# Kernel optimization log

Hardware: AMD Instinct MI355X
Metric: run time of the kernel (lower is better)

## Reference

```python
import jax, jax.numpy as jnp
import numpy as np

E, H = 512, 256  # embed_dim, hidden_dim
B, SQ, SK = 2, 512, 512


def _linear_params(k, fin, fout):
    lim = 1.0 / np.sqrt(fin)
    kw, kb = jax.random.split(k)
    W = jax.random.uniform(kw, (fin, fout), minval=-lim, maxval=lim, dtype=jnp.float32)
    b = jax.random.uniform(kb, (fout,), minval=-lim, maxval=lim, dtype=jnp.float32)
    return W, b


def setup_inputs() -> dict:
    rng = jax.random.key(0)
    ks = jax.random.split(rng, 12)
    query = jax.random.normal(ks[0], (B, SQ, E), dtype=jnp.float32)
    key = jax.random.normal(ks[1], (B, SK, E), dtype=jnp.float32)
    Wqe, bqe = _linear_params(ks[2], E, H)
    Wke, bke = _linear_params(ks[3], E, H)
    W1, b1 = _linear_params(ks[4], 2 * H, H)  # importance_predictor layer 0
    W2, b2 = _linear_params(ks[5], H, H)      # layer 1
    W3, b3 = _linear_params(ks[6], H, H)      # layer 2
    Wf, bf = _linear_params(ks[7], H, 1)      # final importance logit
    Wv1, bv1 = _linear_params(ks[8], 2 * H, H)  # variance_estimator layer 0
    Wv2, bv2 = _linear_params(ks[9], H, 1)      # variance_estimator final
    return {"query": query, "key": key,
            "Wqe": Wqe, "bqe": bqe, "Wke": Wke, "bke": bke,
            "W1": W1, "b1": b1, "W2": W2, "b2": b2, "W3": W3, "b3": b3,
            "Wf": Wf, "bf": bf, "Wv1": Wv1, "bv1": bv1, "Wv2": Wv2, "bv2": bv2}


def reference(query, key, Wqe, bqe, Wke, bke, W1, b1, W2, b2, W3, b3, Wf, bf, Wv1, bv1, Wv2, bv2):
    # Encoders (dropout is identity at eval)
    qf = jax.nn.relu(jnp.einsum('bqe,eh->bqh', query, Wqe) + bqe)  # [B,Sq,H]
    kf = jax.nn.relu(jnp.einsum('bke,eh->bkh', key, Wke) + bke)    # [B,Sk,H]

    # First Linear(2H,H) on cat([q,k]) == q@W1[:H] + k@W1[H:]; broadcast over pairs
    qp = jnp.einsum('bqh,hd->bqd', qf, W1[:H])
    kp = jnp.einsum('bkh,hd->bkd', kf, W1[H:])
    h = jax.nn.relu(qp[:, :, None, :] + kp[:, None, :, :] + b1)  # [B,Sq,Sk,H]
    h = jax.nn.relu(jnp.einsum('bqkh,hd->bqkd', h, W2) + b2)
    h = jax.nn.relu(jnp.einsum('bqkh,hd->bqkd', h, W3) + b3)
    importance_logits = (jnp.einsum('bqkh,ho->bqko', h, Wf) + bf)[..., 0]  # [B,Sq,Sk]

    # Variance head: Linear(2H,H) split the same way, ReLU, Linear, Softplus
    vq = jnp.einsum('bqh,hd->bqd', qf, Wv1[:H])
    vk = jnp.einsum('bkh,hd->bkd', kf, Wv1[H:])
    v = jax.nn.relu(vq[:, :, None, :] + vk[:, None, :, :] + bv1)  # [B,Sq,Sk,H]
    estimated_variance = jax.nn.softplus((jnp.einsum('bqkh,ho->bqko', v, Wv2) + bv2)[..., 0])
    return importance_logits, estimated_variance
```

## Files before the change

kernel.cpp:

```cpp
#include <hip/hip_runtime.h>
#include <hip/hip_bf16.h>
#include <cstdint>
#include <cstddef>
#include <cstring>

#define HDIM 256
#define EDIM 512
#define NB   2
#define NSQ  512
#define NSK  512

typedef _Float16 f16x8 __attribute__((ext_vector_type(8)));
typedef _Float16 h2    __attribute__((ext_vector_type(2)));
typedef __fp16   fp16v2 __attribute__((ext_vector_type(2)));
typedef float    f32x4  __attribute__((ext_vector_type(4)));

#define OFF_W2F  0u
#define OFF_W3F  65536u
#define OFF_WQEF 131072u
#define OFF_WKEF 262144u
#define OFF_WCQ  393216u
#define OFF_WCK  524288u
#define OFF_WV2H 655360u
#define F16_WS_END_BYTES 1312768u

union U8 { f16x8 v; h2 h[4]; };

__device__ __forceinline__ ushort2 f2h2(float x, float y) {
  fp16v2 r = __builtin_amdgcn_cvt_pkrtz(x, y);
  ushort2 u;
  __builtin_memcpy(&u, &r, 4);
  return u;
}
__device__ __forceinline__ float relu_(float x) { return x > 0.f ? x : 0.f; }
__device__ __forceinline__ float softplus_(float x) {
  return fmaxf(x, 0.f) + log1pf(expf(-fabsf(x)));
}

__global__ __launch_bounds__(256) void shuffle_weights(
    const float* __restrict__ Wqe, const float* __restrict__ Wke,
    const float* __restrict__ W1,  const float* __restrict__ Wv1,
    const float* __restrict__ W2,  const float* __restrict__ W3,
    const float* __restrict__ Wv2,
    unsigned short* __restrict__ wsb)
{
  __shared__ float sW[32 * 257];
  const int bx = blockIdx.x;
  const int t = threadIdx.x;
  if (bx == 80) {
    if (t < 64) {
      float a = Wv2[t * 4 + 0], b = Wv2[t * 4 + 1];
      float c = Wv2[t * 4 + 2], d = Wv2[t * 4 + 3];
      ushort2 lo = f2h2(a, b), hi = f2h2(c, d);
      ushort4 o; o.x = lo.x; o.y = lo.y; o.z = hi.x; o.w = hi.y;
      *(ushort4*)&wsb[OFF_WV2H + t * 4] = o;
    }
    return;
  }
  const float* src; unsigned short* dst; int s; int S;
  if      (bx <  8) { src = W2;          dst = wsb + OFF_W2F;           s = bx;      S = 8;  }
  else if (bx < 16) { src = W3;          dst = wsb + OFF_W3F;           s = bx - 8;  S = 8;  }
  else if (bx < 32) { src = Wqe;         dst = wsb + OFF_WQEF;          s = bx - 16; S = 16; }
  else if (bx < 48) { src = Wke;         dst = wsb + OFF_WKEF;          s = bx - 32; S = 16; }
  else if (bx < 56) { src = W1;          dst = wsb + OFF_WCQ;           s = bx - 48; S = 8;  }
  else if (bx < 64) { src = Wv1;         dst = wsb + OFF_WCQ + 65536u;  s = bx - 56; S = 8;  }
  else if (bx < 72) { src = W1 + 65536;  dst = wsb + OFF_WCK;           s = bx - 64; S = 8;  }
  else              { src = Wv1 + 65536; dst = wsb + OFF_WCK + 65536u;  s = bx - 72; S = 8;  }

  const int kbase = s * 32;
  #pragma unroll
  for (int it = 0; it < 8; ++it) {
    const int f4 = it * 256 + t;
    const int row = f4 >> 6, c4 = (f4 & 63) * 4;
    float4 v = *(const float4*)(src + (size_t)(kbase + row) * 256 + c4);
    sW[row * 257 + c4 + 0] = v.x; sW[row * 257 + c4 + 1] = v.y;
    sW[row * 257 + c4 + 2] = v.z; sW[row * 257 + c4 + 3] = v.w;
  }
  __syncthreads();

  const int wave = t >> 6, lane = t & 63;
  const int n_in = lane & 15, k0 = (lane >> 4) * 8;
  for (int tt = wave * 4; tt < wave * 4 + 4; ++tt) {
    const int n = tt * 16 + n_in;
    float x[8];
    #pragma unroll
    for (int j = 0; j < 8; ++j) x[j] = sW[(k0 + j) * 257 + n];
    ushort2 p0 = f2h2(x[0], x[1]), p1 = f2h2(x[2], x[3]);
    ushort2 p2 = f2h2(x[4], x[5]), p3 = f2h2(x[6], x[7]);
    ushort4 lo; lo.x = p0.x; lo.y = p0.y; lo.z = p1.x; lo.w = p1.y;
    ushort4 hi; hi.x = p2.x; hi.y = p2.y; hi.z = p3.x; hi.w = p3.y;
    unsigned short* o = dst + ((size_t)(tt * S + s) * 64 + lane) * 8;
    *(ushort4*)&o[0] = lo; *(ushort4*)&o[4] = hi;
  }
}

__global__ __launch_bounds__(512) void encoder_kernel(
    const float* __restrict__ query, const float* __restrict__ key,
    const float* __restrict__ bqe,   const float* __restrict__ bke,
    const float* __restrict__ b1,    const float* __restrict__ bv1,
    const unsigned short* __restrict__ WqeF, const unsigned short* __restrict__ WkeF,
    const unsigned short* __restrict__ WcqF, const unsigned short* __restrict__ WckF,
    _Float16* __restrict__ Pq, _Float16* __restrict__ Pk)
{
  __shared__ unsigned short sX[16 * 520];
  __shared__ unsigned short sF[16 * 264];
  __shared__ float sBe[256];
  __shared__ float sBc[512];

  const int bx   = blockIdx.x;
  const int side = bx >> 8;
  const int idx  = bx & 255;
  const int rt   = idx >> 2;
  const int nh   = idx & 3;
  const int t    = threadIdx.x;

  const float* Xsrc = side ? key : query;
  const unsigned short* WeF = side ? WkeF : WqeF;
  const unsigned short* WcF = side ? WckF : WcqF;
  _Float16* P = side ? Pk : Pq;

  const int wave = t >> 6, lane = t & 63;
  const int l15 = lane & 15, q4 = lane >> 4;

  const unsigned short* aeb = WeF + ((size_t)(wave * 2) * 16 * 64 + lane) * 8;
  f16x8 afe[2][2];
  #pragma unroll
  for (int ft = 0; ft < 2; ++ft)
    afe[0][ft] = *(const f16x8*)(aeb + ft * 8192);

  {
    const int m = t >> 5, ch = t & 31;
    const float* xr = Xsrc + (size_t)(rt * 16 + m) * EDIM;
    #pragma unroll
    for (int j = 0; j < 4; ++j) {
      const int c = j * 128 + ch * 4;
      float4 v = *(const float4*)(xr + c);
      ushort2 lo = f2h2(v.x, v.y), hi = f2h2(v.z, v.w);
      ushort4 xb; xb.x = lo.x; xb.y = lo.y; xb.z = hi.x; xb.w = hi.y;
      *(ushort4*)&sX[m * 520 + c] = xb;
    }
    if (t < 256) {
      sBe[t]       = side ? bke[t] : bqe[t];
      sBc[t]       = side ? 0.f : b1[t];
      sBc[256 + t] = side ? 0.f : bv1[t];
    }
  }
  __syncthreads();

  f32x4 acc1[2];
  #pragma unroll
  for (int ft = 0; ft < 2; ++ft) acc1[ft] = (f32x4){0.f, 0.f, 0.f, 0.f};

  #pragma unroll
  for (int s = 0; s < 16; ++s) {
    if (s < 15) {
      #pragma unroll
      for (int ft = 0; ft < 2; ++ft)
        afe[(s + 1) & 1][ft] = *(const f16x8*)(aeb + ft * 8192 + (size_t)(s + 1) * 512);
    }
    f16x8 bfr = *(const f16x8*)&sX[l15 * 520 + s * 32 + q4 * 8];
    #pragma unroll
    for (int ft = 0; ft < 2; ++ft)
      acc1[ft] = __builtin_amdgcn_mfma_f32_16x16x32_f16(afe[s & 1][ft], bfr, acc1[ft], 0, 0, 0);
  }

  #pragma unroll
  for (int ft = 0; ft < 2; ++ft) {
    const int tg = wave * 2 + ft;
    const int n0 = tg * 16 + q4 * 4;
    float4 b4 = *(const float4*)&sBe[n0];
    f32x4 a = acc1[ft];
    ushort2 lo = f2h2(relu_(a[0] + b4.x), relu_(a[1] + b4.y));
    ushort2 hi = f2h2(relu_(a[2] + b4.z), relu_(a[3] + b4.w));
    ushort4 h; h.x = lo.x; h.y = lo.y; h.z = hi.x; h.w = hi.y;
    *(ushort4*)&sF[l15 * 264 + n0] = h;
  }
  __syncthreads();

  const int tg2 = nh * 8 + wave;
  const unsigned short* acb = WcF + ((size_t)tg2 * 8 * 64 + lane) * 8;
  f16x8 afc[2];
  afc[0] = *(const f16x8*)(acb);

  f32x4 acc2 = (f32x4){0.f, 0.f, 0.f, 0.f};

  #pragma unroll
  for (int s = 0; s < 8; ++s) {
    if (s < 7)
      afc[(s + 1) & 1] = *(const f16x8*)(acb + (size_t)(s + 1) * 512);
    f16x8 bfr = *(const f16x8*)&sF[l15 * 264 + s * 32 + q4 * 8];
    acc2 = __builtin_amdgcn_mfma_f32_16x16x32_f16(afc[s & 1], bfr, acc2, 0, 0, 0);
  }

  {
    const int n0 = tg2 * 16 + q4 * 4;
    float4 bc = *(const float4*)&sBc[n0];
    const int row = rt * 16 + l15;
    ushort2 lo = f2h2(acc2[0] + bc.x, acc2[1] + bc.y);
    ushort2 hi = f2h2(acc2[2] + bc.z, acc2[3] + bc.w);
    ushort4 o; o.x = lo.x; o.y = lo.y; o.z = hi.x; o.w = hi.y;
    *(ushort4*)((unsigned short*)P + (size_t)row * 512 + n0) = o;
  }
}

__global__ __launch_bounds__(512, 4) void pair_kernel(
    const _Float16* __restrict__ Pq, const _Float16* __restrict__ Pk,
    const unsigned short* __restrict__ W2F, const unsigned short* __restrict__ W3F,
    const float* __restrict__ b2, const float* __restrict__ b3,
    const float* __restrict__ Wf, const float* __restrict__ bfp,
    const unsigned short* __restrict__ Wv2H, const float* __restrict__ bv2p,
    float* __restrict__ out)
{
  __shared__ __align__(16) unsigned char smem[68608];
  unsigned short* sXH = (unsigned short*)smem;
  unsigned short* sH  = (unsigned short*)(smem + 33792);
  float* sRed = (float*)(smem + 67584);

  const int kt = blockIdx.x, qy = blockIdx.y, bz = blockIdx.z;
  const int t = threadIdx.x;
  const _Float16* qpRow = Pq + (size_t)(bz * NSQ + qy) * 512;

  const int wave = t >> 6, lane = t & 63;
  const int l15 = lane & 15, q4 = lane >> 4;
  const int mi = wave >> 2;
  const int ni = wave & 3;

  const unsigned short* a2base = W2F + ((size_t)(ni * 4) * 8 * 64 + lane) * 8;
  const unsigned short* a3base = W3F + ((size_t)(ni * 4) * 8 * 64 + lane) * 8;

  float vp0 = 0.f, vp1 = 0.f;
  {
    const int m   = t >> 3;
    const int sub = t & 7;
    const _Float16* kpRow = Pk + (size_t)(bz * NSK + kt * 64 + m) * 512;
    const f16x8 z8 = {0, 0, 0, 0, 0, 0, 0, 0};
    #pragma unroll
    for (int it = 0; it < 4; ++it) {
      const int c = it * 64 + sub * 8;
      f16x8 q8 = *(const f16x8*)(qpRow + c);
      f16x8 k8 = *(const f16x8*)(kpRow + c);
      f16x8 r  = __builtin_elementwise_max(q8 + k8, z8);
      *(f16x8*)&sXH[m * 264 + c] = r;
      f16x8 a8 = *(const f16x8*)(qpRow + 256 + c);
      f16x8 v8 = *(const f16x8*)(kpRow + 256 + c);
      U8 ar; ar.v = __builtin_elementwise_max(a8 + v8, z8);
      U8 w8; w8.v = *(const f16x8*)((const _Float16*)Wv2H + c);
      vp0 = __builtin_amdgcn_fdot2(ar.h[0], w8.h[0], vp0, false);
      vp1 = __builtin_amdgcn_fdot2(ar.h[1], w8.h[1], vp1, false);
      vp0 = __builtin_amdgcn_fdot2(ar.h[2], w8.h[2], vp0, false);
      vp1 = __builtin_amdgcn_fdot2(ar.h[3], w8.h[3], vp1, false);
    }
  }
  __syncthreads();

  f32x4 acc[4][2];
  #pragma unroll
  for (int ft = 0; ft < 4; ++ft)
    #pragma unroll
    for (int pt = 0; pt < 2; ++pt)
      acc[ft][pt] = (f32x4){0.f, 0.f, 0.f, 0.f};

  #pragma unroll
  for (int s = 0; s < 8; ++s) {
    f16x8 afd[4], bf[2];
    #pragma unroll
    for (int ft = 0; ft < 4; ++ft)
      afd[ft] = *(const f16x8*)(a2base + ft * 4096 + (size_t)s * 512);
    #pragma unroll
    for (int pt = 0; pt < 2; ++pt)
      bf[pt] = *(const f16x8*)&sXH[(mi * 32 + pt * 16 + l15) * 264 + s * 32 + q4 * 8];
    __builtin_amdgcn_s_setprio(1);
    #pragma unroll
    for (int ft = 0; ft < 4; ++ft)
      #pragma unroll
      for (int pt = 0; pt < 2; ++pt)
        acc[ft][pt] = __builtin_amdgcn_mfma_f32_16x16x32_f16(afd[ft], bf[pt], acc[ft][pt], 0, 0, 0);
    __builtin_amdgcn_s_setprio(0);
  }

  #pragma unroll
  for (int ft = 0; ft < 4; ++ft) {
    const int tg = ni * 4 + ft;
    const int n0 = tg * 16 + q4 * 4;
    float4 b4 = *(const float4*)&b2[n0];
    #pragma unroll
    for (int pt = 0; pt < 2; ++pt) {
      const int mr = mi * 32 + pt * 16 + l15;
      f32x4 a = acc[ft][pt];
      ushort2 lo = f2h2(relu_(a[0] + b4.x), relu_(a[1] + b4.y));
      ushort2 hi = f2h2(relu_(a[2] + b4.z), relu_(a[3] + b4.w));
      ushort4 h; h.x = lo.x; h.y = lo.y; h.z = hi.x; h.w = hi.y;
      *(ushort4*)&sH[mr * 264 + n0] = h;
    }
  }
  __syncthreads();

  #pragma unroll
  for (int ft = 0; ft < 4; ++ft)
    #pragma unroll
    for (int pt = 0; pt < 2; ++pt)
      acc[ft][pt] = (f32x4){0.f, 0.f, 0.f, 0.f};

  #pragma unroll
  for (int s = 0; s < 8; ++s) {
    f16x8 afd[4], bf[2];
    #pragma unroll
    for (int ft = 0; ft < 4; ++ft)
      afd[ft] = *(const f16x8*)(a3base + ft * 4096 + (size_t)s * 512);
    #pragma unroll
    for (int pt = 0; pt < 2; ++pt)
      bf[pt] = *(const f16x8*)&sH[(mi * 32 + pt * 16 + l15) * 264 + s * 32 + q4 * 8];
    __builtin_amdgcn_s_setprio(1);
    #pragma unroll
    for (int ft = 0; ft < 4; ++ft)
      #pragma unroll
      for (int pt = 0; pt < 2; ++pt)
        acc[ft][pt] = __builtin_amdgcn_mfma_f32_16x16x32_f16(afd[ft], bf[pt], acc[ft][pt], 0, 0, 0);
    __builtin_amdgcn_s_setprio(0);
  }

  {
    float v = vp0 + vp1;
    v += __shfl_xor(v, 1, 64);
    v += __shfl_xor(v, 2, 64);
    v += __shfl_xor(v, 4, 64);
    if ((t & 7) == 0) {
      const int m = t >> 3;
      const size_t o = (size_t)(bz * NSQ + qy) * NSK + kt * 64 + m;
      out[(size_t)NB * NSQ * NSK + o] = softplus_(v + bv2p[0]);
    }
  }

  {
    float p[2] = {0.f, 0.f};
    #pragma unroll
    for (int ft = 0; ft < 4; ++ft) {
      const int tg = ni * 4 + ft;
      const int n0 = tg * 16 + q4 * 4;
      float4 b4 = *(const float4*)&b3[n0];
      float4 w4 = *(const float4*)&Wf[n0];
      #pragma unroll
      for (int pt = 0; pt < 2; ++pt) {
        f32x4 a = acc[ft][pt];
        p[pt] += relu_(a[0] + b4.x) * w4.x + relu_(a[1] + b4.y) * w4.y
               + relu_(a[2] + b4.z) * w4.z + relu_(a[3] + b4.w) * w4.w;
      }
    }
    #pragma unroll
    for (int pt = 0; pt < 2; ++pt) {
      float v = p[pt];
      v += __shfl_xor(v, 16, 64);
      v += __shfl_xor(v, 32, 64);
      if (lane < 16) sRed[ni * 64 + mi * 32 + pt * 16 + lane] = v;
    }
  }
  __syncthreads();

  if (t < 64) {
    const size_t o = (size_t)(bz * NSQ + qy) * NSK + kt * 64 + t;
    float lg = bfp[0];
    #pragma unroll
    for (int w = 0; w < 4; ++w) lg += sRed[w * 64 + t];
    out[o] = lg;
  }
}

extern "C" void kernel_launch(void* const* d_in, const int* in_sizes, int n_in,
                              void* d_out, int out_size, void* d_ws, size_t ws_size,
                              hipStream_t stream)
{
  (void)in_sizes; (void)n_in; (void)out_size; (void)ws_size;
  const float* query = (const float*)d_in[0];
  const float* key   = (const float*)d_in[1];
  const float* Wqe   = (const float*)d_in[2];
  const float* bqe   = (const float*)d_in[3];
  const float* Wke   = (const float*)d_in[4];
  const float* bke   = (const float*)d_in[5];
  const float* W1    = (const float*)d_in[6];
  const float* b1    = (const float*)d_in[7];
  const float* W2    = (const float*)d_in[8];
  const float* b2    = (const float*)d_in[9];
  const float* W3    = (const float*)d_in[10];
  const float* b3    = (const float*)d_in[11];
  const float* Wf    = (const float*)d_in[12];
  const float* bf    = (const float*)d_in[13];
  const float* Wv1   = (const float*)d_in[14];
  const float* bv1   = (const float*)d_in[15];
  const float* Wv2   = (const float*)d_in[16];
  const float* bv2   = (const float*)d_in[17];

  unsigned short* wsb = (unsigned short*)d_ws;
  _Float16* Pq = (_Float16*)((char*)d_ws + F16_WS_END_BYTES);
  _Float16* Pk = Pq + (size_t)1024 * 512;
  float* out = (float*)d_out;

  shuffle_weights<<<81, 256, 0, stream>>>(Wqe, Wke, W1, Wv1, W2, W3, Wv2, wsb);
  encoder_kernel<<<512, 512, 0, stream>>>(query, key, bqe, bke, b1, bv1,
      wsb + OFF_WQEF, wsb + OFF_WKEF, wsb + OFF_WCQ, wsb + OFF_WCK, Pq, Pk);
  pair_kernel<<<dim3(NSK / 64, NSQ, NB), 512, 0, stream>>>(Pq, Pk,
      wsb + OFF_W2F, wsb + OFF_W3F, b2, b3, Wf, bf, wsb + OFF_WV2H, bv2, out);
}
```

Before: 290.2 us.

## Switch pair-kernel GEMMs to 32x32x16 MFMA with software-pipelined operand loads

The pair kernel's two 256x256 GEMM stages now use 32x32x16 f16 MFMA tiles, two per wave, instead of eight 16x16x32 tiles. The weight-repacking kernel gets a matching 32-wide fragment layout for W2/W3. Weight and LDS operand fragments are prefetched one or two k-steps ahead in a register double-buffer so loads overlap the MFMAs. Larger MFMA tiles reduce instruction count and fragment traffic per FLOP, at the cost of a different accumulator layout in the epilogue and more live registers.

```diff
diff --git a/kernel.cpp b/kernel.cpp
--- a/kernel.cpp
+++ b/kernel.cpp
@@ -14,6 +14,7 @@
 typedef _Float16 h2    __attribute__((ext_vector_type(2)));
 typedef __fp16   fp16v2 __attribute__((ext_vector_type(2)));
 typedef float    f32x4  __attribute__((ext_vector_type(4)));
+typedef float    f32x16 __attribute__((ext_vector_type(16)));
 
 #define OFF_W2F  0u
 #define OFF_W3F  65536u
@@ -79,6 +80,27 @@
   __syncthreads();
 
   const int wave = t >> 6, lane = t & 63;
+
+  if (bx < 16) {
+    const int n_in = lane & 31, kh = (lane >> 5) * 8;
+    #pragma unroll
+    for (int it = 0; it < 4; ++it) {
+      const int tt  = wave * 2 + (it >> 1);
+      const int scl = it & 1;
+      const int k0 = scl * 16 + kh;
+      float x[8];
+      #pragma unroll
+      for (int j = 0; j < 8; ++j) x[j] = sW[(k0 + j) * 257 + tt * 32 + n_in];
+      ushort2 p0 = f2h2(x[0], x[1]), p1 = f2h2(x[2], x[3]);
+      ushort2 p2 = f2h2(x[4], x[5]), p3 = f2h2(x[6], x[7]);
+      ushort4 lo; lo.x = p0.x; lo.y = p0.y; lo.z = p1.x; lo.w = p1.y;
+      ushort4 hi; hi.x = p2.x; hi.y = p2.y; hi.z = p3.x; hi.w = p3.y;
+      unsigned short* o = dst + ((size_t)(tt * 16 + (s * 2 + scl)) * 64 + lane) * 8;
+      *(ushort4*)&o[0] = lo; *(ushort4*)&o[4] = hi;
+    }
+    return;
+  }
+
   const int n_in = lane & 15, k0 = (lane >> 4) * 8;
   for (int tt = wave * 4; tt < wave * 4 + 4; ++tt) {
     const int n = tt * 16 + n_in;
@@ -221,12 +243,15 @@
   const _Float16* qpRow = Pq + (size_t)(bz * NSQ + qy) * 512;
 
   const int wave = t >> 6, lane = t & 63;
-  const int l15 = lane & 15, q4 = lane >> 4;
+  const int l31 = lane & 31, kh = lane >> 5;
   const int mi = wave >> 2;
-  const int ni = wave & 3;
-
-  const unsigned short* a2base = W2F + ((size_t)(ni * 4) * 8 * 64 + lane) * 8;
-  const unsigned short* a3base = W3F + ((size_t)(ni * 4) * 8 * 64 + lane) * 8;
+  const int nj = wave & 3;
+
+  const unsigned short* a2b = W2F + (size_t)(nj * 2) * 8192 + lane * 8;
+  const unsigned short* a3b = W3F + (size_t)(nj * 2) * 8192 + lane * 8;
+
+  f16x8 a0c = *(const f16x8*)(a2b);
+  f16x8 a1c = *(const f16x8*)(a2b + 8192);
 
   float vp0 = 0.f, vp1 = 0.f;
   {
@@ -253,70 +278,71 @@
   }
   __syncthreads();
 
-  f32x4 acc[4][2];
-  #pragma unroll
-  for (int ft = 0; ft < 4; ++ft)
-    #pragma unroll
-    for (int pt = 0; pt < 2; ++pt)
-      acc[ft][pt] = (f32x4){0.f, 0.f, 0.f, 0.f};
-
-  #pragma unroll
-  for (int s = 0; s < 8; ++s) {
-    f16x8 afd[4], bf[2];
-    #pragma unroll
-    for (int ft = 0; ft < 4; ++ft)
-      afd[ft] = *(const f16x8*)(a2base + ft * 4096 + (size_t)s * 512);
-    #pragma unroll
-    for (int pt = 0; pt < 2; ++pt)
-      bf[pt] = *(const f16x8*)&sXH[(mi * 32 + pt * 16 + l15) * 264 + s * 32 + q4 * 8];
+  const int m = mi * 32 + l31;
+  const int brow = m * 264 + kh * 8;
+
+  f32x16 acc0, acc1;
+  #pragma unroll
+  for (int i = 0; i < 16; ++i) { acc0[i] = 0.f; acc1[i] = 0.f; }
+
+  f16x8 bc = *(const f16x8*)&sXH[brow];
+  f16x8 b1f = *(const f16x8*)&sXH[brow + 16];
+
+  #pragma unroll
+  for (int sc = 0; sc < 16; ++sc) {
+    f16x8 a0n, a1n, b2n;
+    if (sc < 15) {
+      a0n = *(const f16x8*)(a2b + (size_t)(sc + 1) * 512);
+      a1n = *(const f16x8*)(a2b + 8192 + (size_t)(sc + 1) * 512);
+    }
+    if (sc < 14)
+      b2n = *(const f16x8*)&sXH[brow + (sc + 2) * 16];
     __builtin_amdgcn_s_setprio(1);
-    #pragma unroll
-    for (int ft = 0; ft < 4; ++ft)
-      #pragma unroll
-      for (int pt = 0; pt < 2; ++pt)
-        acc[ft][pt] = __builtin_amdgcn_mfma_f32_16x16x32_f16(afd[ft], bf[pt], acc[ft][pt], 0, 0, 0);
+    acc0 = __builtin_amdgcn_mfma_f32_32x32x16_f16(a0c, bc, acc0, 0, 0, 0);
+    acc1 = __builtin_amdgcn_mfma_f32_32x32x16_f16(a1c, bc, acc1, 0, 0, 0);
     __builtin_amdgcn_s_setprio(0);
-  }
-
-  #pragma unroll
-  for (int ft = 0; ft < 4; ++ft) {
-    const int tg = ni * 4 + ft;
-    const int n0 = tg * 16 + q4 * 4;
-    float4 b4 = *(const float4*)&b2[n0];
-    #pragma unroll
-    for (int pt = 0; pt < 2; ++pt) {
-      const int mr = mi * 32 + pt * 16 + l15;
-      f32x4 a = acc[ft][pt];
-      ushort2 lo = f2h2(relu_(a[0] + b4.x), relu_(a[1] + b4.y));
-      ushort2 hi = f2h2(relu_(a[2] + b4.z), relu_(a[3] + b4.w));
+    a0c = a0n; a1c = a1n; bc = b1f; b1f = b2n;
+  }
+
+  a0c = *(const f16x8*)(a3b);
+  a1c = *(const f16x8*)(a3b + 8192);
+
+  #pragma unroll
+  for (int ti = 0; ti < 2; ++ti) {
+    const f32x16 a = ti ? acc1 : acc0;
+    const int nb = (nj * 2 + ti) * 32 + kh * 4;
+    #pragma unroll
+    for (int g = 0; g < 4; ++g) {
+      const int n0 = nb + g * 8;
+      float4 b4 = *(const float4*)&b2[n0];
+      ushort2 lo = f2h2(relu_(a[g * 4 + 0] + b4.x), relu_(a[g * 4 + 1] + b4.y));
+      ushort2 hi = f2h2(relu_(a[g * 4 + 2] + b4.z), relu_(a[g * 4 + 3] + b4.w));
       ushort4 h; h.x = lo.x; h.y = lo.y; h.z = hi.x; h.w = hi.y;
-      *(ushort4*)&sH[mr * 264 + n0] = h;
-    }
-  }
-  __syncthreads();
-
-  #pragma unroll
-  for (int ft = 0; ft < 4; ++ft)
-    #pragma unroll
-    for (int pt = 0; pt < 2; ++pt)
-      acc[ft][pt] = (f32x4){0.f, 0.f, 0.f, 0.f};
-
-  #pragma unroll
-  for (int s = 0; s < 8; ++s) {
-    f16x8 afd[4], bf[2];
-    #pragma unroll
-    for (int ft = 0; ft < 4; ++ft)
-      afd[ft] = *(const f16x8*)(a3base + ft * 4096 + (size_t)s * 512);
-    #pragma unroll
-    for (int pt = 0; pt < 2; ++pt)
-      bf[pt] = *(const f16x8*)&sH[(mi * 32 + pt * 16 + l15) * 264 + s * 32 + q4 * 8];
+      *(ushort4*)&sH[m * 264 + n0] = h;
+    }
+  }
+  __syncthreads();
+
+  #pragma unroll
+  for (int i = 0; i < 16; ++i) { acc0[i] = 0.f; acc1[i] = 0.f; }
+
+  bc  = *(const f16x8*)&sH[brow];
+  b1f = *(const f16x8*)&sH[brow + 16];
+
+  #pragma unroll
+  for (int sc = 0; sc < 16; ++sc) {
+    f16x8 a0n, a1n, b2n;
+    if (sc < 15) {
+      a0n = *(const f16x8*)(a3b + (size_t)(sc + 1) * 512);
+      a1n = *(const f16x8*)(a3b + 8192 + (size_t)(sc + 1) * 512);
+    }
+    if (sc < 14)
+      b2n = *(const f16x8*)&sH[brow + (sc + 2) * 16];
     __builtin_amdgcn_s_setprio(1);
-    #pragma unroll
-    for (int ft = 0; ft < 4; ++ft)
-      #pragma unroll
-      for (int pt = 0; pt < 2; ++pt)
-        acc[ft][pt] = __builtin_amdgcn_mfma_f32_16x16x32_f16(afd[ft], bf[pt], acc[ft][pt], 0, 0, 0);
+    acc0 = __builtin_amdgcn_mfma_f32_32x32x16_f16(a0c, bc, acc0, 0, 0, 0);
+    acc1 = __builtin_amdgcn_mfma_f32_32x32x16_f16(a1c, bc, acc1, 0, 0, 0);
     __builtin_amdgcn_s_setprio(0);
+    a0c = a0n; a1c = a1n; bc = b1f; b1f = b2n;
   }
 
   {
@@ -325,34 +351,29 @@
     v += __shfl_xor(v, 2, 64);
     v += __shfl_xor(v, 4, 64);
     if ((t & 7) == 0) {
-      const int m = t >> 3;
-      const size_t o = (size_t)(bz * NSQ + qy) * NSK + kt * 64 + m;
+      const int mr = t >> 3;
+      const size_t o = (size_t)(bz * NSQ + qy) * NSK + kt * 64 + mr;
       out[(size_t)NB * NSQ * NSK + o] = softplus_(v + bv2p[0]);
     }
   }
 
   {
-    float p[2] = {0.f, 0.f};
-    #pragma unroll
-    for (int ft = 0; ft < 4; ++ft) {
-      const int tg = ni * 4 + ft;
-      const int n0 = tg * 16 + q4 * 4;
-      float4 b4 = *(const float4*)&b3[n0];
-      float4 w4 = *(const float4*)&Wf[n0];
+    float p = 0.f;
+    #pragma unroll
+    for (int ti = 0; ti < 2; ++ti) {
+      const f32x16 a = ti ? acc1 : acc0;
+      const int nb = (nj * 2 + ti) * 32 + kh * 4;
       #pragma unroll
-      for (int pt = 0; pt < 2; ++pt) {
-        f32x4 a = acc[ft][pt];
-        p[pt] += relu_(a[0] + b4.x) * w4.x + relu_(a[1] + b4.y) * w4.y
-               + relu_(a[2] + b4.z) * w4.z + relu_(a[3] + b4.w) * w4.w;
+      for (int g = 0; g < 4; ++g) {
+        const int n0 = nb + g * 8;
+        float4 b4 = *(const float4*)&b3[n0];
+        float4 w4 = *(const float4*)&Wf[n0];
+        p += relu_(a[g * 4 + 0] + b4.x) * w4.x + relu_(a[g * 4 + 1] + b4.y) * w4.y
+           + relu_(a[g * 4 + 2] + b4.z) * w4.z + relu_(a[g * 4 + 3] + b4.w) * w4.w;
       }
     }
-    #pragma unroll
-    for (int pt = 0; pt < 2; ++pt) {
-      float v = p[pt];
-      v += __shfl_xor(v, 16, 64);
-      v += __shfl_xor(v, 32, 64);
-      if (lane < 16) sRed[ni * 64 + mi * 32 + pt * 16 + lane] = v;
-    }
+    p += __shfl_xor(p, 32, 64);
+    if (lane < 32) sRed[nj * 64 + m] = p;
   }
   __syncthreads();
 
```

New measurement: 307.5 us. 5.9% more time.

## Split pair tile into two row halves and overlap staging with MFMA GEMMs

Applied to the files above, without the earlier changes.

The pair kernel now handles its 64 key rows as two 32-row halves. Staging of the second half and the epilogue of one half are interleaved with the MFMA GEMMs of the other half, so that global loads and the fp16 conversion can overlap tensor-core work. Each wave now owns two output column tiles across 32 rows instead of a 4x2 wave grid. Weight and B fragments are double-buffered in registers to prefetch the next k-step. This adds more barriers and a second reduction buffer in shared memory, and may change register pressure and occupancy.

```diff
diff --git a/kernel.cpp b/kernel.cpp
--- a/kernel.cpp
+++ b/kernel.cpp
@@ -211,10 +211,11 @@
     const unsigned short* __restrict__ Wv2H, const float* __restrict__ bv2p,
     float* __restrict__ out)
 {
-  __shared__ __align__(16) unsigned char smem[68608];
+  __shared__ __align__(16) unsigned char smem[69632];
   unsigned short* sXH = (unsigned short*)smem;
   unsigned short* sH  = (unsigned short*)(smem + 33792);
-  float* sRed = (float*)(smem + 67584);
+  float* sRed0 = (float*)(smem + 67584);
+  float* sRed1 = (float*)(smem + 68608);
 
   const int kt = blockIdx.x, qy = blockIdx.y, bz = blockIdx.z;
   const int t = threadIdx.x;
@@ -222,21 +223,20 @@
 
   const int wave = t >> 6, lane = t & 63;
   const int l15 = lane & 15, q4 = lane >> 4;
-  const int mi = wave >> 2;
-  const int ni = wave & 3;
-
-  const unsigned short* a2base = W2F + ((size_t)(ni * 4) * 8 * 64 + lane) * 8;
-  const unsigned short* a3base = W3F + ((size_t)(ni * 4) * 8 * 64 + lane) * 8;
-
-  float vp0 = 0.f, vp1 = 0.f;
-  {
-    const int m   = t >> 3;
-    const int sub = t & 7;
+  const int mloc = t >> 4, sub = t & 15;
+
+  const unsigned short* a2base = W2F + ((size_t)(wave * 2) * 8 * 64 + lane) * 8;
+  const unsigned short* a3base = W3F + ((size_t)(wave * 2) * 8 * 64 + lane) * 8;
+
+  const f16x8 z8 = {0, 0, 0, 0, 0, 0, 0, 0};
+
+  auto STAGE = [&](int mb) -> float {
+    const int m = mb + mloc;
     const _Float16* kpRow = Pk + (size_t)(bz * NSK + kt * 64 + m) * 512;
-    const f16x8 z8 = {0, 0, 0, 0, 0, 0, 0, 0};
-    #pragma unroll
-    for (int it = 0; it < 4; ++it) {
-      const int c = it * 64 + sub * 8;
+    float vp0 = 0.f, vp1 = 0.f;
+    #pragma unroll
+    for (int it = 0; it < 2; ++it) {
+      const int c = it * 128 + sub * 8;
       f16x8 q8 = *(const f16x8*)(qpRow + c);
       f16x8 k8 = *(const f16x8*)(kpRow + c);
       f16x8 r  = __builtin_elementwise_max(q8 + k8, z8);
@@ -250,93 +250,71 @@
       vp0 = __builtin_amdgcn_fdot2(ar.h[2], w8.h[2], vp0, false);
       vp1 = __builtin_amdgcn_fdot2(ar.h[3], w8.h[3], vp1, false);
     }
-  }
-  __syncthreads();
-
-  f32x4 acc[4][2];
-  #pragma unroll
-  for (int ft = 0; ft < 4; ++ft)
-    #pragma unroll
-    for (int pt = 0; pt < 2; ++pt)
-      acc[ft][pt] = (f32x4){0.f, 0.f, 0.f, 0.f};
-
-  #pragma unroll
-  for (int s = 0; s < 8; ++s) {
-    f16x8 afd[4], bf[2];
-    #pragma unroll
-    for (int ft = 0; ft < 4; ++ft)
-      afd[ft] = *(const f16x8*)(a2base + ft * 4096 + (size_t)s * 512);
-    #pragma unroll
-    for (int pt = 0; pt < 2; ++pt)
-      bf[pt] = *(const f16x8*)&sXH[(mi * 32 + pt * 16 + l15) * 264 + s * 32 + q4 * 8];
-    __builtin_amdgcn_s_setprio(1);
-    #pragma unroll
-    for (int ft = 0; ft < 4; ++ft)
-      #pragma unroll
-      for (int pt = 0; pt < 2; ++pt)
-        acc[ft][pt] = __builtin_amdgcn_mfma_f32_16x16x32_f16(afd[ft], bf[pt], acc[ft][pt], 0, 0, 0);
-    __builtin_amdgcn_s_setprio(0);
-  }
-
-  #pragma unroll
-  for (int ft = 0; ft < 4; ++ft) {
-    const int tg = ni * 4 + ft;
-    const int n0 = tg * 16 + q4 * 4;
-    float4 b4 = *(const float4*)&b2[n0];
-    #pragma unroll
-    for (int pt = 0; pt < 2; ++pt) {
-      const int mr = mi * 32 + pt * 16 + l15;
-      f32x4 a = acc[ft][pt];
-      ushort2 lo = f2h2(relu_(a[0] + b4.x), relu_(a[1] + b4.y));
-      ushort2 hi = f2h2(relu_(a[2] + b4.z), relu_(a[3] + b4.w));
-      ushort4 h; h.x = lo.x; h.y = lo.y; h.z = hi.x; h.w = hi.y;
-      *(ushort4*)&sH[mr * 264 + n0] = h;
-    }
-  }
-  __syncthreads();
-
-  #pragma unroll
-  for (int ft = 0; ft < 4; ++ft)
-    #pragma unroll
-    for (int pt = 0; pt < 2; ++pt)
-      acc[ft][pt] = (f32x4){0.f, 0.f, 0.f, 0.f};
-
-  #pragma unroll
-  for (int s = 0; s < 8; ++s) {
-    f16x8 afd[4], bf[2];
-    #pragma unroll
-    for (int ft = 0; ft < 4; ++ft)
-      afd[ft] = *(const f16x8*)(a3base + ft * 4096 + (size_t)s * 512);
-    #pragma unroll
-    for (int pt = 0; pt < 2; ++pt)
-      bf[pt] = *(const f16x8*)&sH[(mi * 32 + pt * 16 + l15) * 264 + s * 32 + q4 * 8];
-    __builtin_amdgcn_s_setprio(1);
-    #pragma unroll
-    for (int ft = 0; ft < 4; ++ft)
-      #pragma unroll
-      for (int pt = 0; pt < 2; ++pt)
-        acc[ft][pt] = __builtin_amdgcn_mfma_f32_16x16x32_f16(afd[ft], bf[pt], acc[ft][pt], 0, 0, 0);
-    __builtin_amdgcn_s_setprio(0);
-  }
-
-  {
     float v = vp0 + vp1;
     v += __shfl_xor(v, 1, 64);
     v += __shfl_xor(v, 2, 64);
     v += __shfl_xor(v, 4, 64);
-    if ((t & 7) == 0) {
-      const int m = t >> 3;
-      const size_t o = (size_t)(bz * NSQ + qy) * NSK + kt * 64 + m;
-      out[(size_t)NB * NSQ * NSK + o] = softplus_(v + bv2p[0]);
-    }
-  }
-
-  {
+    v += __shfl_xor(v, 8, 64);
+    return v;
+  };
+
+  auto GEMM = [&](const unsigned short* abase, const unsigned short* Bsrc,
+                  int mb, f32x4 (&acc)[2][2]) {
+    #pragma unroll
+    for (int ft = 0; ft < 2; ++ft)
+      #pragma unroll
+      for (int pt = 0; pt < 2; ++pt)
+        acc[ft][pt] = (f32x4){0.f, 0.f, 0.f, 0.f};
+    f16x8 afd[2][2];
+    afd[0][0] = *(const f16x8*)(abase);
+    afd[0][1] = *(const f16x8*)(abase + 4096);
+    f16x8 bcur[2], bnxt[2];
+    #pragma unroll
+    for (int pt = 0; pt < 2; ++pt)
+      bcur[pt] = *(const f16x8*)&Bsrc[(mb + pt * 16 + l15) * 264 + q4 * 8];
+    #pragma unroll
+    for (int s = 0; s < 8; ++s) {
+      if (s < 7) {
+        afd[(s + 1) & 1][0] = *(const f16x8*)(abase + (size_t)(s + 1) * 512);
+        afd[(s + 1) & 1][1] = *(const f16x8*)(abase + 4096 + (size_t)(s + 1) * 512);
+        #pragma unroll
+        for (int pt = 0; pt < 2; ++pt)
+          bnxt[pt] = *(const f16x8*)&Bsrc[(mb + pt * 16 + l15) * 264 + (s + 1) * 32 + q4 * 8];
+      }
+      __builtin_amdgcn_s_setprio(1);
+      #pragma unroll
+      for (int ft = 0; ft < 2; ++ft)
+        #pragma unroll
+        for (int pt = 0; pt < 2; ++pt)
+          acc[ft][pt] = __builtin_amdgcn_mfma_f32_16x16x32_f16(afd[s & 1][ft], bcur[pt], acc[ft][pt], 0, 0, 0);
+      __builtin_amdgcn_s_setprio(0);
+      #pragma unroll
+      for (int pt = 0; pt < 2; ++pt) bcur[pt] = bnxt[pt];
+    }
+  };
+
+  auto EPI = [&](int mb, f32x4 (&acc)[2][2]) {
+    #pragma unroll
+    for (int ft = 0; ft < 2; ++ft) {
+      const int n0 = (wave * 2 + ft) * 16 + q4 * 4;
+      float4 b4 = *(const float4*)&b2[n0];
+      #pragma unroll
+      for (int pt = 0; pt < 2; ++pt) {
+        const int mr = mb + pt * 16 + l15;
+        f32x4 a = acc[ft][pt];
+        ushort2 lo = f2h2(relu_(a[0] + b4.x), relu_(a[1] + b4.y));
+        ushort2 hi = f2h2(relu_(a[2] + b4.z), relu_(a[3] + b4.w));
+        ushort4 h; h.x = lo.x; h.y = lo.y; h.z = hi.x; h.w = hi.y;
+        *(ushort4*)&sH[mr * 264 + n0] = h;
+      }
+    }
+  };
+
+  auto OUTP = [&](f32x4 (&acc)[2][2], float* sRed) {
     float p[2] = {0.f, 0.f};
     #pragma unroll
-    for (int ft = 0; ft < 4; ++ft) {
-      const int tg = ni * 4 + ft;
-      const int n0 = tg * 16 + q4 * 4;
+    for (int ft = 0; ft < 2; ++ft) {
+      const int n0 = (wave * 2 + ft) * 16 + q4 * 4;
       float4 b4 = *(const float4*)&b3[n0];
       float4 w4 = *(const float4*)&Wf[n0];
       #pragma unroll
@@ -351,17 +329,52 @@
       float v = p[pt];
       v += __shfl_xor(v, 16, 64);
       v += __shfl_xor(v, 32, 64);
-      if (lane < 16) sRed[ni * 64 + mi * 32 + pt * 16 + lane] = v;
-    }
-  }
-  __syncthreads();
-
-  if (t < 64) {
-    const size_t o = (size_t)(bz * NSQ + qy) * NSK + kt * 64 + t;
+      if (lane < 16) sRed[wave * 32 + pt * 16 + lane] = v;
+    }
+  };
+
+  const size_t obase = (size_t)(bz * NSQ + qy) * NSK + kt * 64;
+  const size_t vbase = (size_t)NB * NSQ * NSK + obase;
+
+  f32x4 accA[2][2], accB[2][2];
+
+  float vred0 = STAGE(0);
+  __syncthreads();
+
+  GEMM(a2base, sXH, 0, accA);
+  float vred1 = STAGE(32);
+  __syncthreads();
+
+  EPI(0, accA);
+  GEMM(a2base, sXH, 32, accB);
+  __syncthreads();
+
+  EPI(32, accB);
+  GEMM(a3base, sH, 0, accA);
+  __syncthreads();
+
+  OUTP(accA, sRed0);
+  if (sub == 0)
+    out[vbase + mloc] = softplus_(vred0 + bv2p[0]);
+  GEMM(a3base, sH, 32, accB);
+  __syncthreads();
+
+  if (t < 32) {
     float lg = bfp[0];
     #pragma unroll
-    for (int w = 0; w < 4; ++w) lg += sRed[w * 64 + t];
-    out[o] = lg;
+    for (int w = 0; w < 8; ++w) lg += sRed0[w * 32 + t];
+    out[obase + t] = lg;
+  }
+  OUTP(accB, sRed1);
+  if (sub == 0)
+    out[vbase + 32 + mloc] = softplus_(vred1 + bv2p[0]);
+  __syncthreads();
+
+  if (t < 32) {
+    float lg = bfp[0];
+    #pragma unroll
+    for (int w = 0; w < 8; ++w) lg += sRed1[w * 32 + t];
+    out[obase + 32 + t] = lg;
   }
 }
 
```

Result: slower. 307.9 us (+6.1%).
